# Kernel tuning notes

Measured on AMD Instinct MI355X. Metric: run time of the kernel, lower is better.

The kernel has to match this reference:

```python
import jax, jax.numpy as jnp
import numpy as np

GAMMA = 0.99
ALPHA = 0.01
EPS = 1e-08


def discounted_returns(rewards, gamma):
    # reverse linear recurrence G_t = r_t + gamma * G_{t+1}, scanned over time (dim 0)
    def step(G, r):
        G = r + gamma * G
        return G, G
    G0 = jnp.zeros(rewards.shape[1:], dtype=rewards.dtype)
    _, returns = jax.lax.scan(step, G0, rewards, reverse=True)
    return returns


def setup_inputs() -> dict:
    key = jax.random.key(0)
    k1, k2, k3, k4, k5 = jax.random.split(key, 5)
    T, B = 8192, 4096
    return {
        "rewards": jax.random.normal(k1, (T, B), dtype=jnp.float32),
        "value_estimates": jax.random.normal(k2, (T, B), dtype=jnp.float32),
        "log_probs": jax.random.normal(k3, (T, B), dtype=jnp.float32),
        "entropies": jax.random.uniform(k4, (T, B), dtype=jnp.float32),
        "to_include": jax.random.randint(k5, (T, B), 0, 2) > 0,
    }


def reference(rewards, value_estimates, log_probs, entropies, to_include):
    returns = discounted_returns(rewards, GAMMA)

    mask = to_include.astype(returns.dtype)
    n = jnp.sum(mask)
    # first call: count=1 -> sg=0 -> running stats equal masked batch stats (detached)
    mean = jax.lax.stop_gradient(jnp.sum(returns * mask) / n)
    var = jnp.sum(jnp.square((returns - mean) * mask)) / (n - 1.0)  # torch .std() is unbiased
    std = jax.lax.stop_gradient(jnp.sqrt(var))

    returns = (returns - mean) / (std + EPS)
    advantages = returns - value_estimates

    critic_loss = jnp.sum(jnp.square(advantages) * mask)
    actor_terms = -log_probs * jax.lax.stop_gradient(advantages) - ALPHA * entropies
    actor_loss = jnp.sum(actor_terms * mask)
    return (critic_loss, actor_loss)
```

## Files before the change

### kernel.cpp

```cpp
#include <hip/hip_runtime.h>
#include <hip/hip_cooperative_groups.h>

namespace cg = cooperative_groups;


constexpr int T     = 8192;
constexpr int B     = 4096;
constexpr int B4    = B / 4;
constexpr int BLK   = 256;
constexpr int WAVES = BLK / 64;
constexpr int L     = 32;
constexpr int NC    = T / L;
constexpr int NTILE = NC * 4;
constexpr int GSZ   = 16;
constexpr int NGRP  = NC / GSZ;
constexpr int NTHR  = NTILE * BLK;

constexpr float GAMMA_F = 0.99f;
constexpr double cpow(double g, int n) { double r = 1.0; for (int i = 0; i < n; ++i) r *= g; return r; }
constexpr float G32  = (float)cpow(0.99, L);
constexpr float G512 = (float)cpow(0.99, L * GSZ);

#define COMPC(MJ, GX, RX, VX, LX, ZX, C0X, C1X, C2X, C3X, C4X)   \
    do {                                                         \
        GX = fmaf(GAMMA_F, GX, RX);                              \
        float mm = (MJ);                                         \
        float Gm = mm * GX, vm = mm * VX, lm = mm * LX, mw = mm * w; \
        a[0] += mm; a[1] += Gm;                                  \
        a[2] = fmaf(Gm, GX, a[2]); a[3] = fmaf(Gm, VX, a[3]);    \
        a[4] += vm; a[5] = fmaf(vm, VX, a[5]);                   \
        a[6] = fmaf(lm, GX, a[6]); a[7] += lm;                   \
        a[8] = fmaf(mm, ZX, a[8]); a[9] = fmaf(lm, VX, a[9]);    \
        C0X += mw;                                               \
        C1X = fmaf(mw, GX, C1X);                                 \
        C2X = fmaf(mw, w,  C2X);                                 \
        C3X = fmaf(mw, VX, C3X);                                 \
        C4X = fmaf(mw, LX, C4X);                                 \
    } while (0)

#define MASK_I32 { int4 q = ((const int4*)mp)[e]; \
    m0 = q.x ? 1.f : 0.f; m1 = q.y ? 1.f : 0.f; m2 = q.z ? 1.f : 0.f; m3 = q.w ? 1.f : 0.f; }
#define MASK_U8  { uchar4 q = ((const uchar4*)mp)[e]; \
    m0 = q.x ? 1.f : 0.f; m1 = q.y ? 1.f : 0.f; m2 = q.z ? 1.f : 0.f; m3 = q.w ? 1.f : 0.f; }

#define ITER_BODYC(MASKLOAD)                         \
    _Pragma("unroll 4")                              \
    for (int i = L - 1; i >= 0; --i) {               \
        int e = base + i * B4;                       \
        float4 r = rw[e], v = vv[e], l = lq[e], z = en[e]; \
        float m0, m1, m2, m3;                        \
        MASKLOAD;                                    \
        COMPC(m0, G.x, r.x, v.x, l.x, z.x, c0.x, c1.x, c2.x, c3.x, c4.x); \
        COMPC(m1, G.y, r.y, v.y, l.y, z.y, c0.y, c1.y, c2.y, c3.y, c4.y); \
        COMPC(m2, G.z, r.z, v.z, l.z, z.z, c0.z, c1.z, c2.z, c3.z, c4.z); \
        COMPC(m3, G.w, r.w, v.w, l.w, z.w, c0.w, c1.w, c2.w, c3.w, c4.w); \
        w *= GAMMA_F;                                \
    }

#define COMP(MJ, GX, RX, VX, LX, ZX)                 \
    do {                                             \
        GX = fmaf(GAMMA_F, GX, RX);                  \
        float mm = (MJ);                             \
        float Gm = mm * GX, vm = mm * VX, lm = mm * LX; \
        a[0] += mm; a[1] += Gm;                      \
        a[2] = fmaf(Gm, GX, a[2]);                   \
        a[3] = fmaf(Gm, VX, a[3]);                   \
        a[4] += vm; a[5] = fmaf(vm, VX, a[5]);       \
        a[6] = fmaf(lm, GX, a[6]); a[7] += lm;       \
        a[8] = fmaf(mm, ZX, a[8]);                   \
        a[9] = fmaf(lm, VX, a[9]);                   \
    } while (0)

#define ITER_BODY(MASKLOAD)                          \
    _Pragma("unroll 4")                              \
    for (int i = L - 1; i >= 0; --i) {               \
        int e = base + i * B4;                       \
        float4 r = rw[e], v = vv[e], l = lq[e], z = en[e]; \
        float m0, m1, m2, m3;                        \
        MASKLOAD;                                    \
        COMP(m0, G.x, r.x, v.x, l.x, z.x);           \
        COMP(m1, G.y, r.y, v.y, l.y, z.y);           \
        COMP(m2, G.z, r.z, v.z, l.z, z.z);           \
        COMP(m3, G.w, r.w, v.w, l.w, z.w);           \
    }

__device__ __forceinline__ float4 chunk_scan(const float4* __restrict__ rw, int base) {
    const float g2 = GAMMA_F * GAMMA_F;
    float4 e4 = make_float4(0.f, 0.f, 0.f, 0.f);
    float4 o4 = make_float4(0.f, 0.f, 0.f, 0.f);
    #pragma unroll
    for (int j = L / 2 - 1; j >= 0; --j) {
        float4 ro = rw[base + (2 * j + 1) * B4];
        float4 re = rw[base + (2 * j) * B4];
        o4.x = fmaf(g2, o4.x, ro.x); o4.y = fmaf(g2, o4.y, ro.y);
        o4.z = fmaf(g2, o4.z, ro.z); o4.w = fmaf(g2, o4.w, ro.w);
        e4.x = fmaf(g2, e4.x, re.x); e4.y = fmaf(g2, e4.y, re.y);
        e4.z = fmaf(g2, e4.z, re.z); e4.w = fmaf(g2, e4.w, re.w);
    }
    float4 s;
    s.x = fmaf(GAMMA_F, o4.x, e4.x); s.y = fmaf(GAMMA_F, o4.y, e4.y);
    s.z = fmaf(GAMMA_F, o4.z, e4.z); s.w = fmaf(GAMMA_F, o4.w, e4.w);
    return s;
}

__device__ __forceinline__ float4 chunk_carry(const float4* __restrict__ S,
                                              const float4* __restrict__ Hg,
                                              int c, int b) {
    const int g = c >> 4;
    const int gend = (g << 4) | (GSZ - 1);
    float4 X = make_float4(0.f, 0.f, 0.f, 0.f);
    float w = 1.f;
    for (int cc = c + 1; cc <= gend; ++cc) {
        float4 sv = S[(size_t)cc * B4 + b];
        X.x = fmaf(w, sv.x, X.x); X.y = fmaf(w, sv.y, X.y);
        X.z = fmaf(w, sv.z, X.z); X.w = fmaf(w, sv.w, X.w);
        w *= G32;
    }
    float4 hg = Hg[(size_t)g * B4 + b];
    X.x = fmaf(w, hg.x, X.x); X.y = fmaf(w, hg.y, X.y);
    X.z = fmaf(w, hg.z, X.z); X.w = fmaf(w, hg.w, X.w);
    return X;
}

__device__ __forceinline__ void fold_groups(const float4* __restrict__ S,
                                            float4* __restrict__ Sg, int idx) {
    int g = idx >> 10;
    int bb = idx & 1023;
    float4 X = make_float4(0.f, 0.f, 0.f, 0.f);
    float w = 1.f;
    #pragma unroll
    for (int j = 0; j < GSZ; ++j) {
        float4 sv = S[(size_t)(g * GSZ + j) * B4 + bb];
        X.x = fmaf(w, sv.x, X.x); X.y = fmaf(w, sv.y, X.y);
        X.z = fmaf(w, sv.z, X.z); X.w = fmaf(w, sv.w, X.w);
        w *= G32;
    }
    Sg[(size_t)g * B4 + bb] = X;
}

__device__ __forceinline__ void gscan_col(const float4* __restrict__ Sg,
                                          float4* __restrict__ Hg, int bb) {
    float4 h = make_float4(0.f, 0.f, 0.f, 0.f);
    #pragma unroll
    for (int g = NGRP - 1; g >= 0; --g) {
        Hg[(size_t)g * B4 + bb] = h;
        float4 sv = Sg[(size_t)g * B4 + bb];
        h.x = fmaf(G512, h.x, sv.x); h.y = fmaf(G512, h.y, sv.y);
        h.z = fmaf(G512, h.z, sv.z); h.w = fmaf(G512, h.w, sv.w);
    }
}

__device__ __forceinline__ void finalize(const double s[10], float* out) {
    double n = s[0], SG = s[1], SG2 = s[2], SGv = s[3], Sv = s[4];
    double Sv2 = s[5], SlpG = s[6], Slp = s[7], Sent = s[8], Slpv = s[9];
    double mean = SG / n;
    double css  = SG2 - 2.0 * mean * SG + mean * mean * n;
    double var  = css / (n - 1.0);
    double sd   = sqrt(var);
    double sc   = 1.0 / (sd + 1e-8);
    double critic = sc * sc * css - 2.0 * sc * (SGv - mean * Sv) + Sv2;
    double actor  = -sc * (SlpG - mean * Slp) + Slpv - 0.01 * Sent;
    out[0] = (float)critic;
    out[1] = (float)actor;
}

__device__ __forceinline__ void reduce10_store(double d[10], double* dst,
                                               double shd[WAVES][10], int tid) {
    #pragma unroll
    for (int k = 0; k < 10; ++k)
        #pragma unroll
        for (int off = 32; off; off >>= 1)
            d[k] += __shfl_down(d[k], off);
    int lane = tid & 63, wv = tid >> 6;
    if (lane == 0) {
        #pragma unroll
        for (int k = 0; k < 10; ++k) shd[wv][k] = d[k];
    }
    __syncthreads();
    if (tid == 0) {
        #pragma unroll
        for (int k = 0; k < 10; ++k) {
            double t = shd[0][k];
            #pragma unroll
            for (int ww = 1; ww < WAVES; ++ww) t += shd[ww][k];
            dst[k] = t;
        }
    }
}

__device__ __forceinline__ void reduce4_store(double d[4], double* dst,
                                              double shd[WAVES][10], int tid) {
    #pragma unroll
    for (int k = 0; k < 4; ++k)
        #pragma unroll
        for (int off = 32; off; off >>= 1)
            d[k] += __shfl_down(d[k], off);
    int lane = tid & 63, wv = tid >> 6;
    if (lane == 0) {
        #pragma unroll
        for (int k = 0; k < 4; ++k) shd[wv][k] = d[k];
    }
    __syncthreads();
    if (tid == 0) {
        #pragma unroll
        for (int k = 0; k < 4; ++k) {
            double t = shd[0][k];
            #pragma unroll
            for (int ww = 1; ww < WAVES; ++ww) t += shd[ww][k];
            dst[k] = t;
        }
    }
}

__global__ void __launch_bounds__(BLK, 4) k_all(
    const float4* __restrict__ rw, const float4* __restrict__ vv,
    const float4* __restrict__ lq, const float4* __restrict__ en,
    const void*  __restrict__ mp,
    float4* __restrict__ S, float4* __restrict__ Sg, float4* __restrict__ Hg,
    float4* __restrict__ CF0, float4* __restrict__ CF1, float4* __restrict__ CF2,
    float4* __restrict__ CF3, float4* __restrict__ CF4,
    double* __restrict__ p1, double* __restrict__ p2, float* __restrict__ out)
{
    cg::grid_group grid = cg::this_grid();
    const int tid = threadIdx.x;
    const int bid = blockIdx.x;
    const int c = bid >> 2, s = bid & 3;
    const int b = s * 256 + tid;
    const int base = c * L * B4 + b;
    const size_t gt = (size_t)bid * BLK + tid;

    __shared__ double shd[WAVES][10];
    __shared__ unsigned shp[WAVES];

    unsigned pv = 0;
    {
        const uint4* mq = (const uint4*)mp;
        #pragma unroll
        for (int it = 0; it < 4; ++it) {
            uint4 q = mq[it * BLK + tid];
            pv |= (q.x | q.y | q.z | q.w) & 0xFFFFFF00u;
        }
        #pragma unroll
        for (int off = 32; off; off >>= 1) pv |= __shfl_down(pv, off);
        if ((tid & 63) == 0) shp[tid >> 6] = pv;
        __syncthreads();
        pv = shp[0] | shp[1] | shp[2] | shp[3];
    }
    const bool is32 = (pv == 0);

    {
        float4 G  = make_float4(0.f, 0.f, 0.f, 0.f);
        float4 c0 = G, c1 = G, c2 = G, c3 = G, c4 = G;
        float a[10] = {0.f, 0.f, 0.f, 0.f, 0.f, 0.f, 0.f, 0.f, 0.f, 0.f};
        float w = GAMMA_F;
        if (is32) { ITER_BODYC(MASK_I32); }
        else      { ITER_BODYC(MASK_U8); }

        S[(size_t)c * B4 + b] = G;
        CF0[gt] = c0; CF1[gt] = c1; CF2[gt] = c2; CF3[gt] = c3; CF4[gt] = c4;

        double d[10];
        #pragma unroll
        for (int k = 0; k < 10; ++k) d[k] = (double)a[k];
        reduce10_store(d, p1 + (size_t)bid * 10, shd, tid);
    }
    grid.sync();

    if (bid < NGRP * B4 / BLK) fold_groups(S, Sg, bid * BLK + tid);
    grid.sync();

    if (bid < B4 / BLK) gscan_col(Sg, Hg, bid * BLK + tid);
    grid.sync();

    {
        float4 X = chunk_carry(S, Hg, c, b);
        float4 c0 = CF0[gt], c1 = CF1[gt], c2 = CF2[gt], c3 = CF3[gt], c4 = CF4[gt];
        double hx = X.x, hy = X.y, hz = X.z, hw = X.w;
        double d[4];
        d[0] = hx * c0.x + hy * c0.y + hz * c0.z + hw * c0.w;
        d[1] = 2.0 * (hx * c1.x + hy * c1.y + hz * c1.z + hw * c1.w)
             + (hx * hx * c2.x + hy * hy * c2.y + hz * hz * c2.z + hw * hw * c2.w);
        d[2] = hx * c3.x + hy * c3.y + hz * c3.z + hw * c3.w;
        d[3] = hx * c4.x + hy * c4.y + hz * c4.z + hw * c4.w;
        reduce4_store(d, p2 + (size_t)bid * 4, shd, tid);
    }
    grid.sync();

    if (bid == 0) {
        double d[10];
        #pragma unroll
        for (int k = 0; k < 10; ++k) d[k] = 0.0;
        for (int i = tid; i < NTILE; i += BLK) {
            #pragma unroll
            for (int k = 0; k < 10; ++k) d[k] += p1[(size_t)i * 10 + k];
            d[1] += p2[(size_t)i * 4 + 0];
            d[2] += p2[(size_t)i * 4 + 1];
            d[3] += p2[(size_t)i * 4 + 2];
            d[6] += p2[(size_t)i * 4 + 3];
        }
        #pragma unroll
        for (int k = 0; k < 10; ++k)
            #pragma unroll
            for (int off = 32; off; off >>= 1)
                d[k] += __shfl_down(d[k], off);
        int lane = tid & 63, wv = tid >> 6;
        if (lane == 0) {
            #pragma unroll
            for (int k = 0; k < 10; ++k) shd[wv][k] = d[k];
        }
        __syncthreads();
        if (tid == 0) {
            double sum[10];
            #pragma unroll
            for (int k = 0; k < 10; ++k) {
                double t = shd[0][k];
                #pragma unroll
                for (int ww = 1; ww < WAVES; ++ww) t += shd[ww][k];
                sum[k] = t;
            }
            finalize(sum, out);
        }
    }
}

__global__ void __launch_bounds__(BLK) k_scanf(const float4* __restrict__ rw,
                                               const void* __restrict__ mp,
                                               float4* __restrict__ S,
                                               int* __restrict__ dflag) {
    __shared__ unsigned shp[WAVES];
    const int tid = threadIdx.x, bid = blockIdx.x;
    const int c = bid >> 2, s = bid & 3;
    const int b = s * 256 + tid;
    S[(size_t)c * B4 + b] = chunk_scan(rw, c * L * B4 + b);
    if (bid == NTILE - 1) {
        unsigned pv = 0;
        const uint4* mq = (const uint4*)mp;
        #pragma unroll
        for (int it = 0; it < 4; ++it) {
            uint4 q = mq[it * BLK + tid];
            pv |= (q.x | q.y | q.z | q.w) & 0xFFFFFF00u;
        }
        #pragma unroll
        for (int off = 32; off; off >>= 1) pv |= __shfl_down(pv, off);
        if ((tid & 63) == 0) shp[tid >> 6] = pv;
        __syncthreads();
        if (tid == 0) *dflag = ((shp[0] | shp[1] | shp[2] | shp[3]) == 0) ? 1 : 0;
    }
}

__global__ void __launch_bounds__(BLK) k_foldf(const float4* __restrict__ S,
                                               float4* __restrict__ Sg) {
    fold_groups(S, Sg, blockIdx.x * BLK + threadIdx.x);
}

__global__ void __launch_bounds__(BLK) k_gscanf(const float4* __restrict__ Sg,
                                                float4* __restrict__ Hg) {
    gscan_col(Sg, Hg, blockIdx.x * BLK + threadIdx.x);
}

__global__ void __launch_bounds__(BLK) k_mainf(const float4* __restrict__ rw,
                                               const float4* __restrict__ vv,
                                               const float4* __restrict__ lq,
                                               const float4* __restrict__ en,
                                               const void*  __restrict__ mp,
                                               const int*   __restrict__ dflag,
                                               const float4* __restrict__ S,
                                               const float4* __restrict__ Hg,
                                               double* __restrict__ p1) {
    __shared__ double shd[WAVES][10];
    const int tid = threadIdx.x, bid = blockIdx.x;
    const int c = bid >> 2, s = bid & 3;
    const int b = s * 256 + tid;
    const int base = c * L * B4 + b;
    float4 G = chunk_carry(S, Hg, c, b);
    float a[10] = {0.f, 0.f, 0.f, 0.f, 0.f, 0.f, 0.f, 0.f, 0.f, 0.f};
    if (*dflag) { ITER_BODY(MASK_I32); }
    else        { ITER_BODY(MASK_U8); }
    double d[10];
    #pragma unroll
    for (int k = 0; k < 10; ++k) d[k] = (double)a[k];
    reduce10_store(d, p1 + (size_t)bid * 10, shd, tid);
}

__global__ void __launch_bounds__(BLK) k_finalf(const double* __restrict__ p1,
                                                float* __restrict__ out) {
    __shared__ double shd[WAVES][10];
    const int tid = threadIdx.x;
    double d[10];
    #pragma unroll
    for (int k = 0; k < 10; ++k) d[k] = 0.0;
    for (int i = tid; i < NTILE; i += BLK) {
        #pragma unroll
        for (int k = 0; k < 10; ++k) d[k] += p1[(size_t)i * 10 + k];
    }
    #pragma unroll
    for (int k = 0; k < 10; ++k)
        #pragma unroll
        for (int off = 32; off; off >>= 1)
            d[k] += __shfl_down(d[k], off);
    int lane = tid & 63, wv = tid >> 6;
    if (lane == 0) {
        #pragma unroll
        for (int k = 0; k < 10; ++k) shd[wv][k] = d[k];
    }
    __syncthreads();
    if (tid == 0) {
        double s[10];
        #pragma unroll
        for (int k = 0; k < 10; ++k) {
            double t = shd[0][k];
            #pragma unroll
            for (int ww = 1; ww < WAVES; ++ww) t += shd[ww][k];
            s[k] = t;
        }
        finalize(s, out);
    }
}

extern "C" void kernel_launch(void* const* d_in, const int* in_sizes, int n_in,
                              void* d_out, int out_size, void* d_ws, size_t ws_size,
                              hipStream_t stream) {
    const float4* rw = (const float4*)d_in[0];
    const float4* vv = (const float4*)d_in[1];
    const float4* lq = (const float4*)d_in[2];
    const float4* en = (const float4*)d_in[3];
    const void*   mp = d_in[4];

    char* ws = (char*)d_ws;
    size_t off = 0;
    float4* S   = (float4*)(ws + off); off += (size_t)NC * B4 * 16;
    float4* Sg  = (float4*)(ws + off); off += (size_t)NGRP * B4 * 16;
    float4* Hg  = (float4*)(ws + off); off += (size_t)NGRP * B4 * 16;
    float4* CF0 = (float4*)(ws + off); off += (size_t)NTHR * 16;
    float4* CF1 = (float4*)(ws + off); off += (size_t)NTHR * 16;
    float4* CF2 = (float4*)(ws + off); off += (size_t)NTHR * 16;
    float4* CF3 = (float4*)(ws + off); off += (size_t)NTHR * 16;
    float4* CF4 = (float4*)(ws + off); off += (size_t)NTHR * 16;
    double* p1  = (double*)(ws + off); off += (size_t)NTILE * 10 * 8;
    double* p2  = (double*)(ws + off); off += (size_t)NTILE * 4 * 8;
    int*  dflag = (int*)  (ws + off);
    float* outp = (float*)d_out;

    int dev = 0;
    (void)hipGetDevice(&dev);
    int coop = 0, ncu = 0, maxb = 0;
    (void)hipDeviceGetAttribute(&coop, hipDeviceAttributeCooperativeLaunch, dev);
    (void)hipDeviceGetAttribute(&ncu, hipDeviceAttributeMultiprocessorCount, dev);
    bool use_coop = false;
    if (coop) {
        if (hipOccupancyMaxActiveBlocksPerMultiprocessor(&maxb, k_all, BLK, 0)
                == hipSuccess && (long)maxb * ncu >= NTILE)
            use_coop = true;
    }
    if (use_coop) {
        void* args[] = { (void*)&rw, (void*)&vv, (void*)&lq, (void*)&en,
                         (void*)&mp, (void*)&S, (void*)&Sg, (void*)&Hg,
                         (void*)&CF0, (void*)&CF1, (void*)&CF2, (void*)&CF3,
                         (void*)&CF4, (void*)&p1, (void*)&p2, (void*)&outp };
        if (hipLaunchCooperativeKernel((void*)k_all, dim3(NTILE), dim3(BLK),
                                       args, 0, stream) != hipSuccess)
            use_coop = false;
    }
    if (!use_coop) {
        k_scanf <<<NTILE, BLK, 0, stream>>>(rw, mp, S, dflag);
        k_foldf <<<NGRP * B4 / BLK, BLK, 0, stream>>>(S, Sg);
        k_gscanf<<<B4 / BLK, BLK, 0, stream>>>(Sg, Hg);
        k_mainf <<<NTILE, BLK, 0, stream>>>(rw, vv, lq, en, mp, dflag, S, Hg, p1);
        k_finalf<<<1, BLK, 0, stream>>>(p1, outp);
    }
}
```

Before: 150.3 us.

## Parallelize group-level carry scan and precompute per-chunk carries into buffer

Replaces the single-block-column group scan followed by per-chunk carry recomputation with a phase in which NGRP*4 blocks each recompute the suffix over later groups and then write carries for their 16 chunks into a new H buffer. The final phase then loads its carry directly. This spreads the serial group scan over many more blocks and shortens the critical path between grid syncs. The cost is redundant suffix work across groups and an extra full NC×B4 buffer that is written and read back. Cooperative launch is now skipped when the workspace is too small.

Result: no change. 151.3 us (+0.6%).

```diff
diff --git a/kernel.cpp b/kernel.cpp
--- a/kernel.cpp
+++ b/kernel.cpp
@@ -216,7 +216,7 @@
     const float4* __restrict__ rw, const float4* __restrict__ vv,
     const float4* __restrict__ lq, const float4* __restrict__ en,
     const void*  __restrict__ mp,
-    float4* __restrict__ S, float4* __restrict__ Sg, float4* __restrict__ Hg,
+    float4* __restrict__ S, float4* __restrict__ Sg, float4* __restrict__ H,
     float4* __restrict__ CF0, float4* __restrict__ CF1, float4* __restrict__ CF2,
     float4* __restrict__ CF3, float4* __restrict__ CF4,
     double* __restrict__ p1, double* __restrict__ p2, float* __restrict__ out)
@@ -269,11 +269,28 @@
     if (bid < NGRP * B4 / BLK) fold_groups(S, Sg, bid * BLK + tid);
     grid.sync();
 
-    if (bid < B4 / BLK) gscan_col(Sg, Hg, bid * BLK + tid);
+    if (bid < NGRP * 4) {
+        const int g3 = bid >> 2, s3 = bid & 3;
+        const int col = s3 * 256 + tid;
+        float4 h = make_float4(0.f, 0.f, 0.f, 0.f);
+        for (int gg = NGRP - 1; gg > g3; --gg) {
+            float4 sv = Sg[(size_t)gg * B4 + col];
+            h.x = fmaf(G512, h.x, sv.x); h.y = fmaf(G512, h.y, sv.y);
+            h.z = fmaf(G512, h.z, sv.z); h.w = fmaf(G512, h.w, sv.w);
+        }
+        const int gstart = g3 << 4, gend = gstart + GSZ - 1;
+        #pragma unroll
+        for (int cc = gend; cc >= gstart; --cc) {
+            H[(size_t)cc * B4 + col] = h;
+            float4 sv = S[(size_t)cc * B4 + col];
+            h.x = fmaf(G32, h.x, sv.x); h.y = fmaf(G32, h.y, sv.y);
+            h.z = fmaf(G32, h.z, sv.z); h.w = fmaf(G32, h.w, sv.w);
+        }
+    }
     grid.sync();
 
     {
-        float4 X = chunk_carry(S, Hg, c, b);
+        float4 X = H[(size_t)c * B4 + b];
         float4 c0 = CF0[gt], c1 = CF1[gt], c2 = CF2[gt], c3 = CF3[gt], c4 = CF4[gt];
         double hx = X.x, hy = X.y, hz = X.z, hw = X.w;
         double d[4];
@@ -425,12 +442,14 @@
     const float4* lq = (const float4*)d_in[2];
     const float4* en = (const float4*)d_in[3];
     const void*   mp = d_in[4];
-
     char* ws = (char*)d_ws;
+    float* outp = (float*)d_out;
+
     size_t off = 0;
     float4* S   = (float4*)(ws + off); off += (size_t)NC * B4 * 16;
     float4* Sg  = (float4*)(ws + off); off += (size_t)NGRP * B4 * 16;
     float4* Hg  = (float4*)(ws + off); off += (size_t)NGRP * B4 * 16;
+    float4* H   = (float4*)(ws + off); off += (size_t)NC * B4 * 16;
     float4* CF0 = (float4*)(ws + off); off += (size_t)NTHR * 16;
     float4* CF1 = (float4*)(ws + off); off += (size_t)NTHR * 16;
     float4* CF2 = (float4*)(ws + off); off += (size_t)NTHR * 16;
@@ -438,8 +457,7 @@
     float4* CF4 = (float4*)(ws + off); off += (size_t)NTHR * 16;
     double* p1  = (double*)(ws + off); off += (size_t)NTILE * 10 * 8;
     double* p2  = (double*)(ws + off); off += (size_t)NTILE * 4 * 8;
-    int*  dflag = (int*)  (ws + off);
-    float* outp = (float*)d_out;
+    int*  dflag = (int*)  (ws + off);  off += 64;
 
     int dev = 0;
     (void)hipGetDevice(&dev);
@@ -447,14 +465,14 @@
     (void)hipDeviceGetAttribute(&coop, hipDeviceAttributeCooperativeLaunch, dev);
     (void)hipDeviceGetAttribute(&ncu, hipDeviceAttributeMultiprocessorCount, dev);
     bool use_coop = false;
-    if (coop) {
+    if (coop && off <= ws_size) {
         if (hipOccupancyMaxActiveBlocksPerMultiprocessor(&maxb, k_all, BLK, 0)
                 == hipSuccess && (long)maxb * ncu >= NTILE)
             use_coop = true;
     }
     if (use_coop) {
         void* args[] = { (void*)&rw, (void*)&vv, (void*)&lq, (void*)&en,
-                         (void*)&mp, (void*)&S, (void*)&Sg, (void*)&Hg,
+                         (void*)&mp, (void*)&S, (void*)&Sg, (void*)&H,
                          (void*)&CF0, (void*)&CF1, (void*)&CF2, (void*)&CF3,
                          (void*)&CF4, (void*)&p1, (void*)&p2, (void*)&outp };
         if (hipLaunchCooperativeKernel((void*)k_all, dim3(NTILE), dim3(BLK),
```
